# Performance work log

Hardware: AMD Instinct MI355X
Metric: run time of the kernel (lower is better)

The kernel has to match this reference:

```python
import jax, jax.numpy as jnp
import numpy as np

N_AGENTS = 10
N_ENEMIES = 11
N_ALLIES = 9
H = 64           # rnn_hidden_dim
HYP = 64         # api_hyper_dim
DEPTH = 2        # residual_depth
OWN = 32
EF = 10          # enemy_feats_dim
AF = 10          # ally_feats_dim
N_ACTIONS = 17
BS = 1024


def _hypernet(x, win, bin_, wres, bres, wout, bout):
    # Linear -> ReLU -> DEPTH x (ReLU(Linear)+identity) -> Linear
    h = jax.nn.relu(x @ win + bin_)
    for d in range(DEPTH):
        h = jax.nn.relu(h @ wres[d] + bres[d]) + h
    return h @ wout + bout


def _gru_cell(x, h, wi, wh, bi, bh):
    gi = x @ wi + bi
    gh = h @ wh + bh
    ir, iz, in_ = jnp.split(gi, 3, axis=-1)
    hr, hz, hn = jnp.split(gh, 3, axis=-1)
    r = jax.nn.sigmoid(ir + hr)
    z = jax.nn.sigmoid(iz + hz)
    n = jnp.tanh(in_ + r * hn)
    return (1.0 - z) * n + z * h


def setup_inputs() -> dict:
    key = jax.random.key(0)
    ks = iter(jax.random.split(key, 48))
    def p(shape, s=0.1):
        return jax.random.normal(next(ks), shape, jnp.float32) * s
    N = BS * N_AGENTS
    inp = {
        'own_feats':    p((N, OWN), 1.0),
        'enemy_feats':  p((N * N_ENEMIES, EF), 1.0),
        'ally_feats':   p((N * N_ALLIES, AF), 1.0),
        'hidden_state': p((N, H), 1.0),
        'fc1_w': p((OWN, H)), 'fc1_b': p((H,)),
        'agent_emb': p((N_AGENTS, H)), 'action_emb': p((N_ACTIONS, H)),
        'hen_win': p((EF, HYP)), 'hen_bin': p((HYP,)),
        'hen_wres': p((DEPTH, HYP, HYP)), 'hen_bres': p((DEPTH, HYP)),
        'hen_wout': p((HYP, EF * H)), 'hen_bout': p((EF * H,)),
        'hal_win': p((AF, HYP)), 'hal_bin': p((HYP,)),
        'hal_wres': p((DEPTH, HYP, HYP)), 'hal_bres': p((DEPTH, HYP)),
        'hal_wout': p((HYP, AF * H)), 'hal_bout': p((AF * H,)),
        'gru_wi': p((H, 3 * H)), 'gru_wh': p((H, 3 * H)),
        'gru_bi': p((3 * H,)), 'gru_bh': p((3 * H,)),
        'fc2_w': p((H, 6)), 'fc2_b': p((6,)),
        'how_win': p((EF, HYP)), 'how_bin': p((HYP,)),
        'how_wres': p((DEPTH, HYP, HYP)), 'how_bres': p((DEPTH, HYP)),
        'how_wout': p((HYP, H)), 'how_bout': p((H,)),
        'hob_win': p((EF, HYP)), 'hob_bin': p((HYP,)),
        'hob_wres': p((DEPTH, HYP, HYP)), 'hob_bres': p((DEPTH, HYP)),
        'hob_wout': p((HYP, 1)), 'hob_bout': p((1,)),
        'agent_idx': jax.random.randint(next(ks), (N,), 0, N_AGENTS),
        'last_action_idx': jax.random.randint(next(ks), (N,), 0, N_ACTIONS),
        'bs': BS,
    }
    return inp


def reference(own_feats, enemy_feats, ally_feats, hidden_state,
              fc1_w, fc1_b, agent_emb, action_emb,
              hen_win, hen_bin, hen_wres, hen_bres, hen_wout, hen_bout,
              hal_win, hal_bin, hal_wres, hal_bres, hal_wout, hal_bout,
              gru_wi, gru_wh, gru_bi, gru_bh,
              fc2_w, fc2_b,
              how_win, how_bin, how_wres, how_bres, how_wout, how_bout,
              hob_win, hob_bin, hob_wres, hob_bres, hob_wout, hob_bout,
              agent_idx, last_action_idx, bs):
    N = bs * N_AGENTS
    # own embedding + id embeddings
    emb = own_feats @ fc1_w + fc1_b
    emb = emb + agent_emb[agent_idx] + action_emb[last_action_idx]
    # per-enemy hypernet weights [N*NE, EF, H]; bmm + sum-pool over enemies
    w_en = _hypernet(enemy_feats, hen_win, hen_bin, hen_wres, hen_bres,
                     hen_wout, hen_bout).reshape(-1, EF, H)
    emb_en = jnp.einsum('nf,nfh->nh', enemy_feats, w_en)
    emb_en = emb_en.reshape(N, N_ENEMIES, H).sum(axis=1)
    # per-ally hypernet weights + bmm + sum-pool
    w_al = _hypernet(ally_feats, hal_win, hal_bin, hal_wres, hal_bres,
                     hal_wout, hal_bout).reshape(-1, AF, H)
    emb_al = jnp.einsum('nf,nfh->nh', ally_feats, w_al)
    emb_al = emb_al.reshape(N, N_ALLIES, H).sum(axis=1)
    x = jax.nn.relu(emb + emb_en + emb_al)
    hh = _gru_cell(x, hidden_state.reshape(-1, H), gru_wi, gru_wh, gru_bi, gru_bh)
    q_normal = (hh @ fc2_w + fc2_b).reshape(bs, N_AGENTS, 6)
    # attack-action head: hypernet-generated per-enemy weights/biases
    ow = _hypernet(enemy_feats, how_win, how_bin, how_wres, how_bres,
                   how_wout, how_bout).reshape(N, N_ENEMIES, H)
    ob = _hypernet(enemy_feats, hob_win, hob_bin, hob_wres, hob_bres,
                   hob_wout, hob_bout).reshape(N, N_ENEMIES)
    q_attack = (jnp.einsum('nh,neh->ne', hh, ow) + ob).reshape(bs, N_AGENTS, N_ENEMIES)
    q = jnp.concatenate([q_normal, q_attack], axis=-1)
    return q, hh.reshape(bs, N_AGENTS, H)
```

## Files before the change

### kernel.cpp

```cpp
#include <hip/hip_runtime.h>

#define DI static __device__ __forceinline__

typedef short s16x8 __attribute__((ext_vector_type(8)));
typedef short s16x4 __attribute__((ext_vector_type(4)));
typedef float f32x4 __attribute__((ext_vector_type(4)));

DI unsigned short f2b(float f) {
  union { float f; unsigned u; } v; v.f = f;
  return (unsigned short)((v.u + 0x7FFF + ((v.u >> 16) & 1)) >> 16);
}
DI float b2f(unsigned short s) {
  union { unsigned u; float f; } v; v.u = ((unsigned)s) << 16;
  return v.f;
}
DI f32x4 MFMA(s16x8 a, s16x8 b, f32x4 c) {
  return __builtin_amdgcn_mfma_f32_16x16x32_bf16(a, b, c, 0, 0, 0);
}
DI s16x8 ldg8(const unsigned short* p) { return *(const s16x8*)p; }

#define OFF_WEN   0
#define OFF_WAL   10240
#define OFF_WHOW  20480
#define OFF_WHOB  30720
#define OFF_BGEN  40960
#define OFF_BGAL  83968
#define OFF_WIT   126976
#define OFF_WHT   139264
#define OFF_FC1T  151552
#define OFF_FC2E  153600
#define OFF_HOWT  154624
#define OFF_HOBT  158720
#define SH_END    159744
#define B_EMB_EN  (SH_END*2)
#define B_EMB_AL  (B_EMB_EN + 2621440)
#define B_HB      (B_EMB_AL + 2621440)
#define B_GBF     (B_HB + 40960)

#define HSTR 72
#define PSTR 680

__global__ __launch_bounds__(256) void kprep(
    const float* __restrict__ hen_win, const float* __restrict__ hen_wres,
    const float* __restrict__ hal_win, const float* __restrict__ hal_wres,
    const float* __restrict__ how_win, const float* __restrict__ how_wres,
    const float* __restrict__ hob_win, const float* __restrict__ hob_wres,
    const float* __restrict__ hen_wout, const float* __restrict__ hen_bout,
    const float* __restrict__ hal_wout, const float* __restrict__ hal_bout,
    const float* __restrict__ gru_wi, const float* __restrict__ gru_wh,
    const float* __restrict__ fc1_w, const float* __restrict__ fc2_w,
    const float* __restrict__ how_bout, const float* __restrict__ how_wout,
    const float* __restrict__ hob_wout,
    unsigned short* __restrict__ ws)
{
  const int gid = blockIdx.x * 256 + threadIdx.x;
  const int gsz = gridDim.x * 256;
  for (int i = gid; i < 4 * 10240; i += gsz) {
    int s = i / 10240, idx = i - s * 10240;
    const float* win  = (s == 0) ? hen_win  : (s == 1) ? hal_win  : (s == 2) ? how_win  : hob_win;
    const float* wres = (s == 0) ? hen_wres : (s == 1) ? hal_wres : (s == 2) ? how_wres : hob_wres;
    float v;
    if (idx < 2048) { int n = idx >> 5, k = idx & 31; v = (k < 10) ? win[k*64 + n] : 0.f; }
    else { int r = idx - 2048; int d = r >> 12; int r2 = r & 4095; int n = r2 >> 6, k = r2 & 63;
           v = wres[d*4096 + k*64 + n]; }
    ws[s * 10240 + idx] = f2b(v);
  }
  for (int i = gid; i < 2 * 43008; i += gsz) {
    int s = i / 43008, idx = i - s * 43008;
    const float* wout = s ? hal_wout : hen_wout;
    const float* bout = s ? hal_bout : hen_bout;
    int kl = idx & 31, n = (idx >> 5) & 63, c = idx >> 11;
    int kfg = c * 32 + kl;
    float v = 0.f;
    if (kfg < 640)      { int k = kfg / 10, f = kfg - k * 10; v = wout[k*640 + f*64 + n]; }
    else if (kfg < 650) { v = bout[(kfg - 640)*64 + n]; }
    ws[(s ? OFF_BGAL : OFF_BGEN) + idx] = f2b(v);
  }
  for (int i = gid; i < 2 * 12288; i += gsz) {
    int s = i / 12288, idx = i - s * 12288;
    int n = idx >> 6, k = idx & 63;
    const float* w = s ? gru_wh : gru_wi;
    ws[(s ? OFF_WHT : OFF_WIT) + idx] = f2b(w[k*192 + n]);
  }
  for (int i = gid; i < 2048; i += gsz) { int n = i >> 5, k = i & 31; ws[OFF_FC1T + i] = f2b(fc1_w[k*64 + n]); }
  for (int i = gid; i < 1024; i += gsz) {
    int n = i >> 6, k = i & 63;
    float v = 0.f; if (n < 6) v = fc2_w[k*6 + n]; else if (n == 6) v = how_bout[k];
    ws[OFF_FC2E + i] = f2b(v);
  }
  for (int i = gid; i < 4096; i += gsz) ws[OFF_HOWT + i] = f2b(how_wout[i]);
  for (int i = gid; i < 1024; i += gsz) { int n = i >> 6, k = i & 63; ws[OFF_HOBT + i] = f2b(n == 0 ? hob_wout[k] : 0.f); }
}

DI void run_stack(const unsigned short* x_lds, unsigned short* h_lds,
                  const unsigned short* wg, const float* bin, const float* bres,
                  int NMF, float (&hval)[3][4][4])
{
  const int t = threadIdx.x;
  const int l = t & 63, wv = t >> 6;
  const int lrow = l & 15, lk8 = (l >> 4) * 8, lr4 = (l >> 4) * 4;

  s16x8 bw[4];
  float bb0[4];
#pragma unroll
  for (int nt = 0; nt < 4; nt++) { bw[nt] = ldg8(wg + (nt*16 + lrow)*32 + lk8); bb0[nt] = bin[nt*16 + lrow]; }
#pragma unroll
  for (int i = 0; i < 3; i++) {
    int mf = wv + i * 4;
    if (mf < NMF) {
      s16x8 a = *(const s16x8*)&x_lds[(mf*16 + lrow)*32 + lk8];
#pragma unroll
      for (int nt = 0; nt < 4; nt++) {
        f32x4 d = MFMA(a, bw[nt], f32x4{0.f,0.f,0.f,0.f});
#pragma unroll
        for (int r = 0; r < 4; r++) hval[i][nt][r] = fmaxf(d[r] + bb0[nt], 0.f);
      }
#pragma unroll
      for (int nt = 0; nt < 4; nt++)
#pragma unroll
        for (int r = 0; r < 4; r++)
          h_lds[(mf*16 + lr4 + r)*HSTR + nt*16 + lrow] = f2b(hval[i][nt][r]);
    }
  }
  __syncthreads();
#pragma unroll
  for (int d = 0; d < 2; d++) {
    const unsigned short* wt = wg + 2048 + d * 4096;
    s16x8 bwr[4][2];
    float bbr[4];
#pragma unroll
    for (int nt = 0; nt < 4; nt++) {
      bbr[nt] = bres[d*64 + nt*16 + lrow];
#pragma unroll
      for (int s = 0; s < 2; s++) bwr[nt][s] = ldg8(wt + (nt*16 + lrow)*64 + s*32 + lk8);
    }
    s16x8 af[3][2];
#pragma unroll
    for (int i = 0; i < 3; i++) {
      int mf = wv + i * 4;
      if (mf < NMF) {
#pragma unroll
        for (int s = 0; s < 2; s++) af[i][s] = *(const s16x8*)&h_lds[(mf*16 + lrow)*HSTR + s*32 + lk8];
      }
    }
    __syncthreads();
#pragma unroll
    for (int i = 0; i < 3; i++) {
      int mf = wv + i * 4;
      if (mf < NMF) {
#pragma unroll
        for (int nt = 0; nt < 4; nt++) {
          f32x4 acc = {0.f,0.f,0.f,0.f};
          acc = MFMA(af[i][0], bwr[nt][0], acc);
          acc = MFMA(af[i][1], bwr[nt][1], acc);
#pragma unroll
          for (int r = 0; r < 4; r++) hval[i][nt][r] = fmaxf(acc[r] + bbr[nt], 0.f) + hval[i][nt][r];
        }
#pragma unroll
        for (int nt = 0; nt < 4; nt++)
#pragma unroll
          for (int r = 0; r < 4; r++)
            h_lds[(mf*16 + lr4 + r)*HSTR + nt*16 + lrow] = f2b(hval[i][nt][r]);
      }
    }
    __syncthreads();
  }
}

__global__ __launch_bounds__(256) void khyp_ea(
    const float* __restrict__ en_feats, const float* __restrict__ al_feats,
    const unsigned short* __restrict__ ws,
    const float* __restrict__ en_bin, const float* __restrict__ en_bres,
    const float* __restrict__ al_bin, const float* __restrict__ al_bres,
    float* __restrict__ emb_en, float* __restrict__ emb_al)
{
  __shared__ __align__(16) char smem[38144];
  unsigned short* x_lds = (unsigned short*)smem;
  unsigned short* h_lds = (unsigned short*)(smem + 11264);
  unsigned short* P     = (unsigned short*)smem;
  float* red            = (float*)(smem + PSTR*2*16);

  const int t = threadIdx.x;
  const int l = t & 63, wv = t >> 6;
  const int lrow = l & 15, lk8 = (l >> 4) * 8, lr4 = (l >> 4) * 4;

  const bool en = blockIdx.x < 640;
  const int blk = en ? blockIdx.x : blockIdx.x - 640;
  const int E = en ? 11 : 9;
  const int MT = E * 16;
  const float* feats = (en ? en_feats : al_feats) + blk * MT * 10;
  const unsigned short* Wg = ws + (en ? OFF_WEN : OFF_WAL);
  const unsigned short* Bg = ws + (en ? OFF_BGEN : OFF_BGAL);
  const float* bin  = en ? en_bin  : al_bin;
  const float* bres = en ? en_bres : al_bres;
  float* emb = (en ? emb_en : emb_al) + blk * 1024;

  for (int idx = t; idx < MT * 32; idx += 256) {
    int row = idx >> 5, c = idx & 31;
    x_lds[idx] = (c < 10) ? f2b(feats[row*10 + c]) : (unsigned short)0;
  }
  __syncthreads();

  float hval[3][4][4];
  run_stack(x_lds, h_lds, Wg, bin, bres, E, hval);

  const int a = t >> 4, kg = t & 15, k0 = kg * 4;
  float pacc[4][10];
#pragma unroll
  for (int kk = 0; kk < 4; kk++)
#pragma unroll
    for (int f = 0; f < 10; f++) pacc[kk][f] = 0.f;
  float sx[10];
#pragma unroll
  for (int f = 0; f < 10; f++) sx[f] = 0.f;
  for (int e = 0; e < E; e++) {
    int row = a * E + e;
    s16x4 hv4 = *(const s16x4*)&h_lds[row*HSTR + k0];
    s16x8 xv8 = *(const s16x8*)&x_lds[row*32];
    unsigned xv2 = *(const unsigned*)&x_lds[row*32 + 8];
    float xf[10];
#pragma unroll
    for (int f = 0; f < 8; f++) xf[f] = b2f((unsigned short)xv8[f]);
    xf[8] = b2f((unsigned short)(xv2 & 0xFFFF));
    xf[9] = b2f((unsigned short)(xv2 >> 16));
    float hf[4];
#pragma unroll
    for (int kk = 0; kk < 4; kk++) hf[kk] = b2f((unsigned short)hv4[kk]);
#pragma unroll
    for (int kk = 0; kk < 4; kk++)
#pragma unroll
      for (int f = 0; f < 10; f++) pacc[kk][f] += hf[kk] * xf[f];
    if (kg == 0) {
#pragma unroll
      for (int f = 0; f < 10; f++) sx[f] += xf[f];
    }
  }
  __syncthreads();
#pragma unroll
  for (int kk = 0; kk < 4; kk++)
#pragma unroll
    for (int f = 0; f < 10; f++)
      P[a*PSTR + (k0 + kk)*10 + f] = f2b(pacc[kk][f]);
  if (kg == 0) {
#pragma unroll
    for (int f = 0; f < 10; f++) P[a*PSTR + 640 + f] = f2b(sx[f]);
  }
  for (int i = t; i < 352; i += 256) { int a2 = i / 22, c = i - (i/22)*22; P[a2*PSTR + 650 + c] = 0; }
  __syncthreads();

  f32x4 gacc[4];
#pragma unroll
  for (int nt = 0; nt < 4; nt++) gacc[nt] = f32x4{0.f,0.f,0.f,0.f};
  int c = wv;
  s16x8 afr = *(const s16x8*)&P[lrow*PSTR + c*32 + lk8];
  s16x8 bfr[4];
#pragma unroll
  for (int nt = 0; nt < 4; nt++) bfr[nt] = ldg8(Bg + (c*64 + nt*16 + lrow)*32 + lk8);
  while (c < 21) {
    int cn = c + 4;
    s16x8 afn = afr;
    s16x8 bfn[4] = {bfr[0], bfr[1], bfr[2], bfr[3]};
    if (cn < 21) {
      afn = *(const s16x8*)&P[lrow*PSTR + cn*32 + lk8];
#pragma unroll
      for (int nt = 0; nt < 4; nt++) bfn[nt] = ldg8(Bg + (cn*64 + nt*16 + lrow)*32 + lk8);
    }
#pragma unroll
    for (int nt = 0; nt < 4; nt++) gacc[nt] = MFMA(afr, bfr[nt], gacc[nt]);
    afr = afn;
#pragma unroll
    for (int nt = 0; nt < 4; nt++) bfr[nt] = bfn[nt];
    c = cn;
  }
#pragma unroll
  for (int nt = 0; nt < 4; nt++)
#pragma unroll
    for (int r = 0; r < 4; r++)
      red[(wv*16 + lr4 + r)*64 + nt*16 + lrow] = gacc[nt][r];
  __syncthreads();
#pragma unroll
  for (int rep = 0; rep < 4; rep++) {
    int idx = t + rep * 256;
    int aa = idx >> 6, j = idx & 63;
    emb[aa*64 + j] = red[aa*64 + j] + red[(16+aa)*64 + j] + red[(32+aa)*64 + j] + red[(48+aa)*64 + j];
  }
}

__global__ __launch_bounds__(256) void kfused(
    const float* __restrict__ own, const float* __restrict__ agent_emb,
    const float* __restrict__ action_emb,
    const int* __restrict__ agent_idx, const int* __restrict__ last_action,
    const float* __restrict__ emb_en, const float* __restrict__ emb_al,
    const float* __restrict__ hidden,
    const unsigned short* __restrict__ ws,
    const float* __restrict__ fc1_b, const float* __restrict__ bi,
    const float* __restrict__ bh, const float* __restrict__ fc2_b,
    float* __restrict__ qout, float* __restrict__ hhout,
    unsigned short* __restrict__ g_bf, float* __restrict__ hb)
{
  __shared__ unsigned short own_lds[16*32];
  __shared__ unsigned short x_lds[16*HSTR];
  __shared__ unsigned short hp_lds[16*HSTR];
  __shared__ unsigned short hh_lds[16*HSTR];
  const int t = threadIdx.x;
  const int l = t & 63, wv = t >> 6;
  const int lrow = l & 15, lk8 = (l >> 4) * 8, lr4 = (l >> 4) * 4;
  const int n0 = blockIdx.x * 16;

  const unsigned short* fc1T = ws + OFF_FC1T;
  const unsigned short* wiT  = ws + OFF_WIT;
  const unsigned short* whT  = ws + OFF_WHT;
  const unsigned short* howT = ws + OFF_HOWT;
  const unsigned short* fc2e = ws + OFF_FC2E;

  for (int i = t; i < 512; i += 256) own_lds[i] = f2b(own[n0*32 + i]);
  for (int i = t; i < 1024; i += 256) hp_lds[(i >> 6)*HSTR + (i & 63)] = f2b(hidden[n0*64 + i]);
  __syncthreads();

  const int j = wv * 16 + lrow;
  {
    s16x8 a0 = *(const s16x8*)&own_lds[lrow*32 + lk8];
    s16x8 b0 = ldg8(fc1T + (wv*16 + lrow)*32 + lk8);
    f32x4 c0 = MFMA(a0, b0, f32x4{0.f,0.f,0.f,0.f});
    float fb = fc1_b[j];
#pragma unroll
    for (int r = 0; r < 4; r++) {
      int aa = lr4 + r; int n = n0 + aa;
      int ai = agent_idx[n], la = last_action[n];
      float v = c0[r] + fb + agent_emb[ai*64 + j] + action_emb[la*64 + j]
              + emb_en[n*64 + j] + emb_al[n*64 + j];
      x_lds[aa*HSTR + j] = f2b(fmaxf(v, 0.f));
    }
  }
  __syncthreads();

  {
    s16x8 xa[2], ha[2];
#pragma unroll
    for (int s = 0; s < 2; s++) {
      xa[s] = *(const s16x8*)&x_lds[lrow*HSTR + s*32 + lk8];
      ha[s] = *(const s16x8*)&hp_lds[lrow*HSTR + s*32 + lk8];
    }
    f32x4 gi[3], gh[3];
#pragma unroll
    for (int g3 = 0; g3 < 3; g3++) { gi[g3] = f32x4{0.f,0.f,0.f,0.f}; gh[g3] = f32x4{0.f,0.f,0.f,0.f}; }
#pragma unroll
    for (int g3 = 0; g3 < 3; g3++) {
      int tl = wv + g3 * 4;
#pragma unroll
      for (int s = 0; s < 2; s++) {
        gi[g3] = MFMA(xa[s], ldg8(wiT + (tl*16 + lrow)*64 + s*32 + lk8), gi[g3]);
        gh[g3] = MFMA(ha[s], ldg8(whT + (tl*16 + lrow)*64 + s*32 + lk8), gh[g3]);
      }
    }
    float bir = bi[j], biz = bi[64 + j], bin_ = bi[128 + j];
    float bhr = bh[j], bhz = bh[64 + j], bhn = bh[128 + j];
#pragma unroll
    for (int r = 0; r < 4; r++) {
      int aa = lr4 + r; int n = n0 + aa;
      float rr = 1.f / (1.f + __expf(-(gi[0][r] + bir + gh[0][r] + bhr)));
      float zz = 1.f / (1.f + __expf(-(gi[1][r] + biz + gh[1][r] + bhz)));
      float nn = tanhf(gi[2][r] + bin_ + rr * (gh[2][r] + bhn));
      float hp = hidden[n*64 + j];
      float hhv = (1.f - zz) * nn + zz * hp;
      hhout[n*64 + j] = hhv;
      hh_lds[aa*HSTR + j] = f2b(hhv);
    }
  }
  __syncthreads();

  {
    s16x8 hha[2];
#pragma unroll
    for (int s = 0; s < 2; s++) hha[s] = *(const s16x8*)&hh_lds[lrow*HSTR + s*32 + lk8];
    f32x4 gc = {0.f,0.f,0.f,0.f};
#pragma unroll
    for (int s = 0; s < 2; s++) gc = MFMA(hha[s], ldg8(howT + (wv*16 + lrow)*64 + s*32 + lk8), gc);
#pragma unroll
    for (int r = 0; r < 4; r++) g_bf[(n0 + lr4 + r)*64 + wv*16 + lrow] = f2b(gc[r]);
    if (wv == 0) {
      f32x4 qc = {0.f,0.f,0.f,0.f};
#pragma unroll
      for (int s = 0; s < 2; s++) qc = MFMA(hha[s], ldg8(fc2e + lrow*64 + s*32 + lk8), qc);
#pragma unroll
      for (int r = 0; r < 4; r++) {
        int n = n0 + lr4 + r;
        if (lrow < 6)       qout[n*17 + lrow] = qc[r] + fc2_b[lrow];
        else if (lrow == 6) hb[n] = qc[r];
      }
    }
  }
}

__global__ __launch_bounds__(256) void kattack(
    const float* __restrict__ en_feats, const unsigned short* __restrict__ ws,
    const float* __restrict__ how_bin, const float* __restrict__ how_bres,
    const float* __restrict__ hob_bin, const float* __restrict__ hob_bres,
    const unsigned short* __restrict__ g_bf, const float* __restrict__ hb,
    const float* __restrict__ hob_bout, float* __restrict__ qout)
{
  __shared__ __align__(16) unsigned short x_lds[176*32];
  __shared__ __align__(16) unsigned short h_lds[176*HSTR];
  __shared__ float qB[176];
  const int t = threadIdx.x;
  const int l = t & 63, wv = t >> 6;
  const int lrow = l & 15, lk8 = (l >> 4) * 8, lr4 = (l >> 4) * 4;
  const int blk = blockIdx.x;
  const float* feats = en_feats + blk * 1760;

  for (int idx = t; idx < 176*32; idx += 256) {
    int row = idx >> 5, c = idx & 31;
    x_lds[idx] = (c < 10) ? f2b(feats[row*10 + c]) : (unsigned short)0;
  }
  __syncthreads();

  float hval[3][4][4];
  run_stack(x_lds, h_lds, ws + OFF_WHOB, hob_bin, hob_bres, 11, hval);

#pragma unroll
  for (int i = 0; i < 3; i++) {
    int mf = wv + i * 4;
    if (mf < 11) {
      s16x8 aa0 = *(const s16x8*)&h_lds[(mf*16 + lrow)*HSTR + lk8];
      s16x8 aa1 = *(const s16x8*)&h_lds[(mf*16 + lrow)*HSTR + 32 + lk8];
      f32x4 qc = {0.f,0.f,0.f,0.f};
      qc = MFMA(aa0, ldg8(ws + OFF_HOBT + lrow*64 + lk8), qc);
      qc = MFMA(aa1, ldg8(ws + OFF_HOBT + lrow*64 + 32 + lk8), qc);
      if (lrow == 0) {
#pragma unroll
        for (int r = 0; r < 4; r++) qB[mf*16 + lr4 + r] = qc[r];
      }
    }
  }
  __syncthreads();

  run_stack(x_lds, h_lds, ws + OFF_WHOW, how_bin, how_bres, 11, hval);

  float hob_b0 = hob_bout[0];
#pragma unroll
  for (int i = 0; i < 3; i++) {
    int mf = wv + i * 4;
    if (mf < 11) {
      s16x8 aa0 = *(const s16x8*)&h_lds[(mf*16 + lrow)*HSTR + lk8];
      s16x8 aa1 = *(const s16x8*)&h_lds[(mf*16 + lrow)*HSTR + 32 + lk8];
      f32x4 qc = {0.f,0.f,0.f,0.f};
      qc = MFMA(aa0, ldg8(g_bf + (blk*16 + lrow)*64 + lk8), qc);
      qc = MFMA(aa1, ldg8(g_bf + (blk*16 + lrow)*64 + 32 + lk8), qc);
#pragma unroll
      for (int r = 0; r < 4; r++) {
        int row = mf*16 + lr4 + r;
        int ag = row / 11;
        if (ag == lrow) {
          int e = row - ag * 11;
          int n = blk*16 + ag;
          qout[n*17 + 6 + e] = qc[r] + qB[row] + hb[n] + hob_b0;
        }
      }
    }
  }
}

extern "C" void kernel_launch(void* const* d_in, const int* in_sizes, int n_in,
                              void* d_out, int out_size, void* d_ws, size_t ws_size,
                              hipStream_t stream)
{
  (void)in_sizes; (void)n_in; (void)out_size; (void)ws_size;
  const float* own        = (const float*)d_in[0];
  const float* enemy      = (const float*)d_in[1];
  const float* ally       = (const float*)d_in[2];
  const float* hidden     = (const float*)d_in[3];
  const float* fc1_w      = (const float*)d_in[4];
  const float* fc1_b      = (const float*)d_in[5];
  const float* agent_emb  = (const float*)d_in[6];
  const float* action_emb = (const float*)d_in[7];
  const float* hen_win  = (const float*)d_in[8];  const float* hen_bin  = (const float*)d_in[9];
  const float* hen_wres = (const float*)d_in[10]; const float* hen_bres = (const float*)d_in[11];
  const float* hen_wout = (const float*)d_in[12]; const float* hen_bout = (const float*)d_in[13];
  const float* hal_win  = (const float*)d_in[14]; const float* hal_bin  = (const float*)d_in[15];
  const float* hal_wres = (const float*)d_in[16]; const float* hal_bres = (const float*)d_in[17];
  const float* hal_wout = (const float*)d_in[18]; const float* hal_bout = (const float*)d_in[19];
  const float* gru_wi = (const float*)d_in[20];   const float* gru_wh = (const float*)d_in[21];
  const float* gru_bi = (const float*)d_in[22];   const float* gru_bh = (const float*)d_in[23];
  const float* fc2_w  = (const float*)d_in[24];   const float* fc2_b  = (const float*)d_in[25];
  const float* how_win  = (const float*)d_in[26]; const float* how_bin  = (const float*)d_in[27];
  const float* how_wres = (const float*)d_in[28]; const float* how_bres = (const float*)d_in[29];
  const float* how_wout = (const float*)d_in[30]; const float* how_bout = (const float*)d_in[31];
  const float* hob_win  = (const float*)d_in[32]; const float* hob_bin  = (const float*)d_in[33];
  const float* hob_wres = (const float*)d_in[34]; const float* hob_bres = (const float*)d_in[35];
  const float* hob_wout = (const float*)d_in[36]; const float* hob_bout = (const float*)d_in[37];
  const int* agent_idx   = (const int*)d_in[38];
  const int* last_action = (const int*)d_in[39];

  unsigned short* ws = (unsigned short*)d_ws;
  float* emb_en = (float*)((char*)d_ws + B_EMB_EN);
  float* emb_al = (float*)((char*)d_ws + B_EMB_AL);
  float* hb     = (float*)((char*)d_ws + B_HB);
  unsigned short* g_bf = (unsigned short*)((char*)d_ws + B_GBF);

  float* q  = (float*)d_out;
  float* hh = q + 1024*10*17;

  kprep<<<128, 256, 0, stream>>>(hen_win, hen_wres, hal_win, hal_wres,
      how_win, how_wres, hob_win, hob_wres,
      hen_wout, hen_bout, hal_wout, hal_bout,
      gru_wi, gru_wh, fc1_w, fc2_w, how_bout, how_wout, hob_wout, ws);
  khyp_ea<<<1280, 256, 0, stream>>>(enemy, ally, ws,
      hen_bin, hen_bres, hal_bin, hal_bres, emb_en, emb_al);
  kfused<<<640, 256, 0, stream>>>(own, agent_emb, action_emb, agent_idx, last_action,
      emb_en, emb_al, hidden, ws, fc1_b, gru_bi, gru_bh, fc2_b, q, hh, g_bf, hb);
  kattack<<<640, 256, 0, stream>>>(enemy, ws, how_bin, how_bres, hob_bin, hob_bres,
      g_bf, hb, hob_bout, q);
}
```

Baseline: 80.51 us.

## Halve agents per block in hypernet kernels to double grid and occupancy

The enemy/ally hypernet kernel and the attack kernel now handle 8 agents per block instead of 16, which doubles the grid and shrinks shared memory. Launch bounds now request 5 blocks per CU. The residual stack is templated on tile count, and some barriers between LDS reads and writes are removed because each wave only touches its own rows. The generated-weight contraction now has each wave own a 16-column slice with two accumulators, replacing the cross-wave reduction buffer, and the qB shared array is replaced by a lane shuffle. The aim is more resident waves and less synchronisation, at the cost of loading weights more often per agent and a padded M tile (96 rows for 88).

Result: slower. 164.1 us (+103.9%).

```diff
diff --git a/kernel.cpp b/kernel.cpp
--- a/kernel.cpp
+++ b/kernel.cpp
@@ -3,7 +3,6 @@
 #define DI static __device__ __forceinline__
 
 typedef short s16x8 __attribute__((ext_vector_type(8)));
-typedef short s16x4 __attribute__((ext_vector_type(4)));
 typedef float f32x4 __attribute__((ext_vector_type(4)));
 
 DI unsigned short f2b(float f) {
@@ -37,6 +36,7 @@
 #define B_HB      (B_EMB_AL + 2621440)
 #define B_GBF     (B_HB + 40960)
 
+#define XSTR 40
 #define HSTR 72
 #define PSTR 680
 
@@ -92,69 +92,28 @@
   for (int i = gid; i < 1024; i += gsz) { int n = i >> 6, k = i & 63; ws[OFF_HOBT + i] = f2b(n == 0 ? hob_wout[k] : 0.f); }
 }
 
+template<int NT>
 DI void run_stack(const unsigned short* x_lds, unsigned short* h_lds,
                   const unsigned short* wg, const float* bin, const float* bres,
-                  int NMF, float (&hval)[3][4][4])
+                  float (&hval)[2][4][4])
 {
   const int t = threadIdx.x;
   const int l = t & 63, wv = t >> 6;
   const int lrow = l & 15, lk8 = (l >> 4) * 8, lr4 = (l >> 4) * 4;
-
-  s16x8 bw[4];
-  float bb0[4];
-#pragma unroll
-  for (int nt = 0; nt < 4; nt++) { bw[nt] = ldg8(wg + (nt*16 + lrow)*32 + lk8); bb0[nt] = bin[nt*16 + lrow]; }
-#pragma unroll
-  for (int i = 0; i < 3; i++) {
-    int mf = wv + i * 4;
-    if (mf < NMF) {
-      s16x8 a = *(const s16x8*)&x_lds[(mf*16 + lrow)*32 + lk8];
-#pragma unroll
-      for (int nt = 0; nt < 4; nt++) {
-        f32x4 d = MFMA(a, bw[nt], f32x4{0.f,0.f,0.f,0.f});
-#pragma unroll
-        for (int r = 0; r < 4; r++) hval[i][nt][r] = fmaxf(d[r] + bb0[nt], 0.f);
-      }
-#pragma unroll
-      for (int nt = 0; nt < 4; nt++)
-#pragma unroll
-        for (int r = 0; r < 4; r++)
-          h_lds[(mf*16 + lr4 + r)*HSTR + nt*16 + lrow] = f2b(hval[i][nt][r]);
-    }
-  }
-  __syncthreads();
-#pragma unroll
-  for (int d = 0; d < 2; d++) {
-    const unsigned short* wt = wg + 2048 + d * 4096;
-    s16x8 bwr[4][2];
-    float bbr[4];
-#pragma unroll
-    for (int nt = 0; nt < 4; nt++) {
-      bbr[nt] = bres[d*64 + nt*16 + lrow];
-#pragma unroll
-      for (int s = 0; s < 2; s++) bwr[nt][s] = ldg8(wt + (nt*16 + lrow)*64 + s*32 + lk8);
-    }
-    s16x8 af[3][2];
-#pragma unroll
-    for (int i = 0; i < 3; i++) {
+  {
+    s16x8 bw[4]; float bb0[4];
+#pragma unroll
+    for (int nt = 0; nt < 4; nt++) { bw[nt] = ldg8(wg + (nt*16 + lrow)*32 + lk8); bb0[nt] = bin[nt*16 + lrow]; }
+#pragma unroll
+    for (int i = 0; i < 2; i++) {
       int mf = wv + i * 4;
-      if (mf < NMF) {
-#pragma unroll
-        for (int s = 0; s < 2; s++) af[i][s] = *(const s16x8*)&h_lds[(mf*16 + lrow)*HSTR + s*32 + lk8];
-      }
-    }
-    __syncthreads();
-#pragma unroll
-    for (int i = 0; i < 3; i++) {
-      int mf = wv + i * 4;
-      if (mf < NMF) {
+      if (mf < NT) {
+        s16x8 a = *(const s16x8*)&x_lds[(mf*16 + lrow)*XSTR + lk8];
 #pragma unroll
         for (int nt = 0; nt < 4; nt++) {
-          f32x4 acc = {0.f,0.f,0.f,0.f};
-          acc = MFMA(af[i][0], bwr[nt][0], acc);
-          acc = MFMA(af[i][1], bwr[nt][1], acc);
-#pragma unroll
-          for (int r = 0; r < 4; r++) hval[i][nt][r] = fmaxf(acc[r] + bbr[nt], 0.f) + hval[i][nt][r];
+          f32x4 d = MFMA(a, bw[nt], f32x4{0.f,0.f,0.f,0.f});
+#pragma unroll
+          for (int r = 0; r < 4; r++) hval[i][nt][r] = fmaxf(d[r] + bb0[nt], 0.f);
         }
 #pragma unroll
         for (int nt = 0; nt < 4; nt++)
@@ -163,126 +122,135 @@
             h_lds[(mf*16 + lr4 + r)*HSTR + nt*16 + lrow] = f2b(hval[i][nt][r]);
       }
     }
-    __syncthreads();
-  }
-}
-
-__global__ __launch_bounds__(256) void khyp_ea(
+  }
+#pragma unroll
+  for (int d = 0; d < 2; d++) {
+    const unsigned short* wt = wg + 2048 + d * 4096;
+    s16x8 bwr[4][2]; float bbr[4];
+#pragma unroll
+    for (int nt = 0; nt < 4; nt++) {
+      bbr[nt] = bres[d*64 + nt*16 + lrow];
+      bwr[nt][0] = ldg8(wt + (nt*16 + lrow)*64 + lk8);
+      bwr[nt][1] = ldg8(wt + (nt*16 + lrow)*64 + 32 + lk8);
+    }
+#pragma unroll
+    for (int i = 0; i < 2; i++) {
+      int mf = wv + i * 4;
+      if (mf < NT) {
+        s16x8 af0 = *(const s16x8*)&h_lds[(mf*16 + lrow)*HSTR + lk8];
+        s16x8 af1 = *(const s16x8*)&h_lds[(mf*16 + lrow)*HSTR + 32 + lk8];
+#pragma unroll
+        for (int nt = 0; nt < 4; nt++) {
+          f32x4 acc = MFMA(af0, bwr[nt][0], f32x4{0.f,0.f,0.f,0.f});
+          acc = MFMA(af1, bwr[nt][1], acc);
+#pragma unroll
+          for (int r = 0; r < 4; r++) hval[i][nt][r] = fmaxf(acc[r] + bbr[nt], 0.f) + hval[i][nt][r];
+        }
+#pragma unroll
+        for (int nt = 0; nt < 4; nt++)
+#pragma unroll
+          for (int r = 0; r < 4; r++)
+            h_lds[(mf*16 + lr4 + r)*HSTR + nt*16 + lrow] = f2b(hval[i][nt][r]);
+      }
+    }
+  }
+}
+
+template<int E, int NT>
+DI void hyp_body(const float* __restrict__ feats,
+                 const unsigned short* __restrict__ Wg, const unsigned short* __restrict__ Bg,
+                 const float* __restrict__ bin, const float* __restrict__ bres,
+                 float* __restrict__ emb,
+                 unsigned short* x_lds, unsigned short* h_lds, unsigned short* P)
+{
+  const int t = threadIdx.x;
+  const int l = t & 63, wv = t >> 6;
+  const int lrow = l & 15, lk8 = (l >> 4) * 8, lr4 = (l >> 4) * 4;
+  constexpr int MT = E * 8;
+
+  for (int idx = t; idx < 96*32; idx += 256) {
+    int row = idx >> 5, c = idx & 31;
+    float v = (c < 10 && row < MT) ? feats[row*10 + c] : 0.f;
+    x_lds[row*XSTR + c] = f2b(v);
+  }
+  __syncthreads();
+
+  float hval[2][4][4];
+  run_stack<NT>(x_lds, h_lds, Wg, bin, bres, hval);
+  __syncthreads();
+
+  const int a = t >> 5, k2 = (t & 31) * 2, fx = t & 31;
+  float p0[10], p1[10], sxv = 0.f;
+#pragma unroll
+  for (int f = 0; f < 10; f++) { p0[f] = 0.f; p1[f] = 0.f; }
+#pragma unroll
+  for (int e = 0; e < E; e++) {
+    int row = a * E + e;
+    const unsigned short* xr = x_lds + row * XSTR;
+    s16x8 xv8 = *(const s16x8*)xr;
+    unsigned xv2 = *(const unsigned*)(xr + 8);
+    float xf[10];
+#pragma unroll
+    for (int f = 0; f < 8; f++) xf[f] = b2f((unsigned short)xv8[f]);
+    xf[8] = b2f((unsigned short)(xv2 & 0xFFFF));
+    xf[9] = b2f((unsigned short)(xv2 >> 16));
+    unsigned hp = *(const unsigned*)&h_lds[row*HSTR + k2];
+    float h0 = b2f((unsigned short)(hp & 0xFFFF));
+    float h1 = b2f((unsigned short)(hp >> 16));
+#pragma unroll
+    for (int f = 0; f < 10; f++) { p0[f] += h0 * xf[f]; p1[f] += h1 * xf[f]; }
+    if (fx < 10) sxv += xf[fx];
+  }
+  __syncthreads();
+  unsigned* Pw = (unsigned*)(P + a*PSTR + k2*10);
+#pragma unroll
+  for (int j = 0; j < 5; j++) Pw[j]     = (unsigned)f2b(p0[2*j]) | ((unsigned)f2b(p0[2*j+1]) << 16);
+#pragma unroll
+  for (int j = 0; j < 5; j++) Pw[5 + j] = (unsigned)f2b(p1[2*j]) | ((unsigned)f2b(p1[2*j+1]) << 16);
+  if (fx < 10) P[a*PSTR + 640 + fx] = f2b(sxv);
+  __syncthreads();
+
+  const int arow = lrow & 7;
+  const unsigned short* Bw = Bg + (wv*16 + lrow)*32 + lk8;
+  f32x4 acc0 = {0.f,0.f,0.f,0.f}, acc1 = {0.f,0.f,0.f,0.f};
+  s16x8 aC = *(const s16x8*)&P[arow*PSTR + lk8];
+  s16x8 bC = ldg8(Bw);
+#pragma unroll
+  for (int c = 0; c < 21; c++) {
+    s16x8 aN = aC, bN = bC;
+    if (c < 20) {
+      aN = *(const s16x8*)&P[arow*PSTR + (c+1)*32 + lk8];
+      bN = ldg8(Bw + (c+1)*2048);
+    }
+    if (c & 1) acc1 = MFMA(aC, bC, acc1); else acc0 = MFMA(aC, bC, acc0);
+    aC = aN; bC = bN;
+  }
+  if (l < 32) {
+#pragma unroll
+    for (int r = 0; r < 4; r++)
+      emb[(lr4 + r)*64 + wv*16 + lrow] = acc0[r] + acc1[r];
+  }
+}
+
+__global__ __launch_bounds__(256, 5) void khyp_ea(
     const float* __restrict__ en_feats, const float* __restrict__ al_feats,
     const unsigned short* __restrict__ ws,
     const float* __restrict__ en_bin, const float* __restrict__ en_bres,
     const float* __restrict__ al_bin, const float* __restrict__ al_bres,
     float* __restrict__ emb_en, float* __restrict__ emb_al)
 {
-  __shared__ __align__(16) char smem[38144];
+  __shared__ __align__(16) char smem[21504];
   unsigned short* x_lds = (unsigned short*)smem;
-  unsigned short* h_lds = (unsigned short*)(smem + 11264);
+  unsigned short* h_lds = (unsigned short*)(smem + 7680);
   unsigned short* P     = (unsigned short*)smem;
-  float* red            = (float*)(smem + PSTR*2*16);
-
-  const int t = threadIdx.x;
-  const int l = t & 63, wv = t >> 6;
-  const int lrow = l & 15, lk8 = (l >> 4) * 8, lr4 = (l >> 4) * 4;
-
-  const bool en = blockIdx.x < 640;
-  const int blk = en ? blockIdx.x : blockIdx.x - 640;
-  const int E = en ? 11 : 9;
-  const int MT = E * 16;
-  const float* feats = (en ? en_feats : al_feats) + blk * MT * 10;
-  const unsigned short* Wg = ws + (en ? OFF_WEN : OFF_WAL);
-  const unsigned short* Bg = ws + (en ? OFF_BGEN : OFF_BGAL);
-  const float* bin  = en ? en_bin  : al_bin;
-  const float* bres = en ? en_bres : al_bres;
-  float* emb = (en ? emb_en : emb_al) + blk * 1024;
-
-  for (int idx = t; idx < MT * 32; idx += 256) {
-    int row = idx >> 5, c = idx & 31;
-    x_lds[idx] = (c < 10) ? f2b(feats[row*10 + c]) : (unsigned short)0;
-  }
-  __syncthreads();
-
-  float hval[3][4][4];
-  run_stack(x_lds, h_lds, Wg, bin, bres, E, hval);
-
-  const int a = t >> 4, kg = t & 15, k0 = kg * 4;
-  float pacc[4][10];
-#pragma unroll
-  for (int kk = 0; kk < 4; kk++)
-#pragma unroll
-    for (int f = 0; f < 10; f++) pacc[kk][f] = 0.f;
-  float sx[10];
-#pragma unroll
-  for (int f = 0; f < 10; f++) sx[f] = 0.f;
-  for (int e = 0; e < E; e++) {
-    int row = a * E + e;
-    s16x4 hv4 = *(const s16x4*)&h_lds[row*HSTR + k0];
-    s16x8 xv8 = *(const s16x8*)&x_lds[row*32];
-    unsigned xv2 = *(const unsigned*)&x_lds[row*32 + 8];
-    float xf[10];
-#pragma unroll
-    for (int f = 0; f < 8; f++) xf[f] = b2f((unsigned short)xv8[f]);
-    xf[8] = b2f((unsigned short)(xv2 & 0xFFFF));
-    xf[9] = b2f((unsigned short)(xv2 >> 16));
-    float hf[4];
-#pragma unroll
-    for (int kk = 0; kk < 4; kk++) hf[kk] = b2f((unsigned short)hv4[kk]);
-#pragma unroll
-    for (int kk = 0; kk < 4; kk++)
-#pragma unroll
-      for (int f = 0; f < 10; f++) pacc[kk][f] += hf[kk] * xf[f];
-    if (kg == 0) {
-#pragma unroll
-      for (int f = 0; f < 10; f++) sx[f] += xf[f];
-    }
-  }
-  __syncthreads();
-#pragma unroll
-  for (int kk = 0; kk < 4; kk++)
-#pragma unroll
-    for (int f = 0; f < 10; f++)
-      P[a*PSTR + (k0 + kk)*10 + f] = f2b(pacc[kk][f]);
-  if (kg == 0) {
-#pragma unroll
-    for (int f = 0; f < 10; f++) P[a*PSTR + 640 + f] = f2b(sx[f]);
-  }
-  for (int i = t; i < 352; i += 256) { int a2 = i / 22, c = i - (i/22)*22; P[a2*PSTR + 650 + c] = 0; }
-  __syncthreads();
-
-  f32x4 gacc[4];
-#pragma unroll
-  for (int nt = 0; nt < 4; nt++) gacc[nt] = f32x4{0.f,0.f,0.f,0.f};
-  int c = wv;
-  s16x8 afr = *(const s16x8*)&P[lrow*PSTR + c*32 + lk8];
-  s16x8 bfr[4];
-#pragma unroll
-  for (int nt = 0; nt < 4; nt++) bfr[nt] = ldg8(Bg + (c*64 + nt*16 + lrow)*32 + lk8);
-  while (c < 21) {
-    int cn = c + 4;
-    s16x8 afn = afr;
-    s16x8 bfn[4] = {bfr[0], bfr[1], bfr[2], bfr[3]};
-    if (cn < 21) {
-      afn = *(const s16x8*)&P[lrow*PSTR + cn*32 + lk8];
-#pragma unroll
-      for (int nt = 0; nt < 4; nt++) bfn[nt] = ldg8(Bg + (cn*64 + nt*16 + lrow)*32 + lk8);
-    }
-#pragma unroll
-    for (int nt = 0; nt < 4; nt++) gacc[nt] = MFMA(afr, bfr[nt], gacc[nt]);
-    afr = afn;
-#pragma unroll
-    for (int nt = 0; nt < 4; nt++) bfr[nt] = bfn[nt];
-    c = cn;
-  }
-#pragma unroll
-  for (int nt = 0; nt < 4; nt++)
-#pragma unroll
-    for (int r = 0; r < 4; r++)
-      red[(wv*16 + lr4 + r)*64 + nt*16 + lrow] = gacc[nt][r];
-  __syncthreads();
-#pragma unroll
-  for (int rep = 0; rep < 4; rep++) {
-    int idx = t + rep * 256;
-    int aa = idx >> 6, j = idx & 63;
-    emb[aa*64 + j] = red[aa*64 + j] + red[(16+aa)*64 + j] + red[(32+aa)*64 + j] + red[(48+aa)*64 + j];
+  if (blockIdx.x < 1280) {
+    int blk = blockIdx.x;
+    hyp_body<11,6>(en_feats + blk*880, ws + OFF_WEN, ws + OFF_BGEN,
+                   en_bin, en_bres, emb_en + blk*512, x_lds, h_lds, P);
+  } else {
+    int blk = blockIdx.x - 1280;
+    hyp_body<9,5>(al_feats + blk*720, ws + OFF_WAL, ws + OFF_BGAL,
+                  al_bin, al_bres, emb_al + blk*512, x_lds, h_lds, P);
   }
 }
 
@@ -392,68 +360,63 @@
   }
 }
 
-__global__ __launch_bounds__(256) void kattack(
+__global__ __launch_bounds__(256, 5) void kattack(
     const float* __restrict__ en_feats, const unsigned short* __restrict__ ws,
     const float* __restrict__ how_bin, const float* __restrict__ how_bres,
     const float* __restrict__ hob_bin, const float* __restrict__ hob_bres,
     const unsigned short* __restrict__ g_bf, const float* __restrict__ hb,
     const float* __restrict__ hob_bout, float* __restrict__ qout)
 {
-  __shared__ __align__(16) unsigned short x_lds[176*32];
-  __shared__ __align__(16) unsigned short h_lds[176*HSTR];
-  __shared__ float qB[176];
+  __shared__ __align__(16) char smem[21504];
+  unsigned short* x_lds = (unsigned short*)smem;
+  unsigned short* h_lds = (unsigned short*)(smem + 7680);
   const int t = threadIdx.x;
   const int l = t & 63, wv = t >> 6;
   const int lrow = l & 15, lk8 = (l >> 4) * 8, lr4 = (l >> 4) * 4;
   const int blk = blockIdx.x;
-  const float* feats = en_feats + blk * 1760;
-
-  for (int idx = t; idx < 176*32; idx += 256) {
+  const float* feats = en_feats + blk * 880;
+
+  for (int idx = t; idx < 96*32; idx += 256) {
     int row = idx >> 5, c = idx & 31;
-    x_lds[idx] = (c < 10) ? f2b(feats[row*10 + c]) : (unsigned short)0;
-  }
-  __syncthreads();
-
-  float hval[3][4][4];
-  run_stack(x_lds, h_lds, ws + OFF_WHOB, hob_bin, hob_bres, 11, hval);
-
-#pragma unroll
-  for (int i = 0; i < 3; i++) {
+    float v = (c < 10 && row < 88) ? feats[row*10 + c] : 0.f;
+    x_lds[row*XSTR + c] = f2b(v);
+  }
+  __syncthreads();
+
+  float hval[2][4][4];
+  run_stack<6>(x_lds, h_lds, ws + OFF_WHOB, hob_bin, hob_bres, hval);
+  float qb[2][4];
+#pragma unroll
+  for (int i = 0; i < 2; i++) {
     int mf = wv + i * 4;
-    if (mf < 11) {
-      s16x8 aa0 = *(const s16x8*)&h_lds[(mf*16 + lrow)*HSTR + lk8];
-      s16x8 aa1 = *(const s16x8*)&h_lds[(mf*16 + lrow)*HSTR + 32 + lk8];
-      f32x4 qc = {0.f,0.f,0.f,0.f};
-      qc = MFMA(aa0, ldg8(ws + OFF_HOBT + lrow*64 + lk8), qc);
-      qc = MFMA(aa1, ldg8(ws + OFF_HOBT + lrow*64 + 32 + lk8), qc);
-      if (lrow == 0) {
-#pragma unroll
-        for (int r = 0; r < 4; r++) qB[mf*16 + lr4 + r] = qc[r];
-      }
-    }
-  }
-  __syncthreads();
-
-  run_stack(x_lds, h_lds, ws + OFF_WHOW, how_bin, how_bres, 11, hval);
+    if (mf < 6) {
+      s16x8 a0 = *(const s16x8*)&h_lds[(mf*16 + lrow)*HSTR + lk8];
+      s16x8 a1 = *(const s16x8*)&h_lds[(mf*16 + lrow)*HSTR + 32 + lk8];
+      f32x4 qc = MFMA(a0, ldg8(ws + OFF_HOBT + lrow*64 + lk8), f32x4{0.f,0.f,0.f,0.f});
+      qc = MFMA(a1, ldg8(ws + OFF_HOBT + lrow*64 + 32 + lk8), qc);
+#pragma unroll
+      for (int r = 0; r < 4; r++) qb[i][r] = qc[r];
+    }
+  }
+  run_stack<6>(x_lds, h_lds, ws + OFF_WHOW, how_bin, how_bres, hval);
 
   float hob_b0 = hob_bout[0];
 #pragma unroll
-  for (int i = 0; i < 3; i++) {
+  for (int i = 0; i < 2; i++) {
     int mf = wv + i * 4;
-    if (mf < 11) {
-      s16x8 aa0 = *(const s16x8*)&h_lds[(mf*16 + lrow)*HSTR + lk8];
-      s16x8 aa1 = *(const s16x8*)&h_lds[(mf*16 + lrow)*HSTR + 32 + lk8];
-      f32x4 qc = {0.f,0.f,0.f,0.f};
-      qc = MFMA(aa0, ldg8(g_bf + (blk*16 + lrow)*64 + lk8), qc);
-      qc = MFMA(aa1, ldg8(g_bf + (blk*16 + lrow)*64 + 32 + lk8), qc);
+    if (mf < 6) {
+      s16x8 a0 = *(const s16x8*)&h_lds[(mf*16 + lrow)*HSTR + lk8];
+      s16x8 a1 = *(const s16x8*)&h_lds[(mf*16 + lrow)*HSTR + 32 + lk8];
+      f32x4 qc = MFMA(a0, ldg8(g_bf + ((long)blk*8 + lrow)*64 + lk8), f32x4{0.f,0.f,0.f,0.f});
+      qc = MFMA(a1, ldg8(g_bf + ((long)blk*8 + lrow)*64 + 32 + lk8), qc);
 #pragma unroll
       for (int r = 0; r < 4; r++) {
         int row = mf*16 + lr4 + r;
         int ag = row / 11;
-        if (ag == lrow) {
-          int e = row - ag * 11;
-          int n = blk*16 + ag;
-          qout[n*17 + 6 + e] = qc[r] + qB[row] + hb[n] + hob_b0;
+        float qBv = __shfl(qb[i][r], l & 48, 64);
+        if (row < 88 && ag == lrow) {
+          int n = blk*8 + ag;
+          qout[n*17 + 6 + (row - ag*11)] = qc[r] + qBv + hb[n] + hob_b0;
         }
       }
     }
@@ -504,10 +467,10 @@
       how_win, how_wres, hob_win, hob_wres,
       hen_wout, hen_bout, hal_wout, hal_bout,
       gru_wi, gru_wh, fc1_w, fc2_w, how_bout, how_wout, hob_wout, ws);
-  khyp_ea<<<1280, 256, 0, stream>>>(enemy, ally, ws,
+  khyp_ea<<<2560, 256, 0, stream>>>(enemy, ally, ws,
       hen_bin, hen_bres, hal_bin, hal_bres, emb_en, emb_al);
   kfused<<<640, 256, 0, stream>>>(own, agent_emb, action_emb, agent_idx, last_action,
       emb_en, emb_al, hidden, ws, fc1_b, gru_bi, gru_bh, fc2_b, q, hh, g_bf, hb);
-  kattack<<<640, 256, 0, stream>>>(enemy, ws, how_bin, how_bres, hob_bin, hob_bres,
+  kattack<<<1280, 256, 0, stream>>>(enemy, ws, how_bin, how_bres, hob_bin, hob_bres,
       g_bf, hb, hob_bout, q);
 }
```
